# Performance work log

Measured on AMD Instinct MI355X. Metric: run time of the kernel, lower is better.

The kernel has to match this reference:

```python
import jax, jax.numpy as jnp
import numpy as np

B, P, M, H = 64, 50, 512, 64
E = 400
HYP = (1000, 2)
NEG_SLOPE = 0.01

def _leaky(x):
    return jnp.where(x >= 0, x, NEG_SLOPE * x)

def setup_inputs() -> dict:
    key = jax.random.key(0)
    ks = jax.random.split(key, 20)
    def lin(kw, kb, fi, fo):
        s = 1.0 / np.sqrt(fi)
        return (jax.random.uniform(kw, (fi, fo), jnp.float32, -s, s),
                jax.random.uniform(kb, (fo,), jnp.float32, -s, s))
    W1, b1 = lin(ks[0], ks[1], P * M, P * H)
    W2, b2 = lin(ks[2], ks[3], P * H, 2 * P * H)
    W3, b3 = lin(ks[4], ks[5], 2 * P * H, 4 * P * H)
    Wc1, bc1 = lin(ks[6], ks[7], 4 * H, 2 * H)
    Wc2, bc2 = lin(ks[8], ks[9], 2 * H, 2 * H)
    Wf1, bf1 = lin(ks[10], ks[11], 2 * H, H)
    Wf2 = jax.random.normal(ks[12], (H, int(np.prod(HYP))), jnp.float32) * 1e-7
    bf2 = jnp.full((int(np.prod(HYP)),), -10.0, jnp.float32)
    b = jax.random.normal(ks[13], (B, P, M), jnp.float32)
    edge_index = jax.random.randint(ks[14], (B, 2, E), 0, P, jnp.int32)
    return {"b": b, "edge_index": edge_index,
            "W1": W1, "b1": b1, "W2": W2, "b2": b2, "W3": W3, "b3": b3,
            "Wc1": Wc1, "bc1": bc1, "Wc2": Wc2, "bc2": bc2,
            "Wf1": Wf1, "bf1": bf1, "Wf2": Wf2, "bf2": bf2}

def _gcn(x, src, dst, norm, W, bias):
    # x: (P, Fin); symmetric-normalized sum aggregation at dst (PyG GCNConv)
    h = x @ W
    return jax.ops.segment_sum(h[src] * norm[:, None], dst, num_segments=P) + bias

def _per_sample(nodes, ei, Wc1, bc1, Wc2, bc2, Wf1, bf1, Wf2, bf2):
    loops = jnp.arange(P, dtype=ei.dtype)
    src = jnp.concatenate([ei[0], loops])
    dst = jnp.concatenate([ei[1], loops])
    deg = jax.ops.segment_sum(jnp.ones(src.shape[0], nodes.dtype), dst, num_segments=P)
    dinv = jnp.where(deg > 0, jax.lax.rsqrt(deg), 0.0)
    norm = dinv[src] * dinv[dst]
    h = _leaky(_gcn(nodes, src, dst, norm, Wc1, bc1))
    h = _leaky(_gcn(h, src, dst, norm, Wc2, bc2))
    pooled = h.mean(axis=0)                       # global_mean_pool, single graph
    z = _leaky(pooled @ Wf1 + bf1)
    z = z @ Wf2 + bf2
    return z.reshape(HYP)

def reference(b, edge_index, W1, b1, W2, b2, W3, b3, Wc1, bc1, Wc2, bc2, Wf1, bf1, Wf2, bf2):
    x = b.reshape(B, -1)
    x = _leaky(x @ W1 + b1)
    x = _leaky(x @ W2 + b2)
    x = x @ W3 + b3                               # encoder ends with Linear
    nodes = x.reshape(B, P, 4 * H)
    hyp = jax.vmap(lambda n, e: _per_sample(n, e, Wc1, bc1, Wc2, bc2, Wf1, bf1, Wf2, bf2))(nodes, edge_index)
    hyp = jnp.cumsum(hyp, axis=1)
    return jax.nn.sigmoid(hyp)
```

## Files before the change

kernel.cpp:

```cpp
#include <hip/hip_runtime.h>
#include <math.h>

typedef __attribute__((ext_vector_type(8))) short short8;
typedef __attribute__((ext_vector_type(4))) float floatx4;

constexpr int kB  = 64;
constexpr int kP  = 50;
constexpr int kE  = 400;
constexpr int kF1 = 128;
constexpr int kH  = 64;
constexpr int kNT = 2000;
constexpr int kNEDGE = kE + kP;

__device__ __forceinline__ unsigned short f2bf(float f) {
    union { float f; unsigned u; } v; v.f = f;
    unsigned u = v.u;
    u += 0x7fffu + ((u >> 16) & 1u);
    return (unsigned short)(u >> 16);
}

__device__ __forceinline__ float leakyf(float v) { return v >= 0.f ? v : 0.01f * v; }

__global__ __launch_bounds__(256) void gemm_bf16(
    const float* __restrict__ A, const float* __restrict__ W, float* __restrict__ C,
    int Mr, int N, int K, int kchunk)
{
    __shared__ unsigned short lds_a[64 * 40];
    __shared__ unsigned short lds_w[64 * 40];

    const int t  = threadIdx.x;
    const int n0 = blockIdx.x * 64;
    const int m0 = blockIdx.y * 64;
    const int k0 = blockIdx.z * kchunk;
    const int kend = k0 + kchunk;
    const bool accumulate = (gridDim.z > 1);

    const int ar = t >> 2;
    const int ac = (t & 3) * 8;
    const int wc = t & 63;
    const int wr = (t >> 6) * 8;

    const int wave = t >> 6;
    const int lane = t & 63;
    const int lrow = lane & 15;
    const int quad = lane >> 4;

    floatx4 acc[4];
#pragma unroll
    for (int c = 0; c < 4; ++c) acc[c] = (floatx4)0.f;

    for (int kk = k0; kk < kend; kk += 32) {
        {
            const float4* ap = reinterpret_cast<const float4*>(
                &A[(size_t)(m0 + ar) * K + kk + ac]);
            float4 v0 = ap[0], v1 = ap[1];
            unsigned short* dst = &lds_a[ar * 40 + ac];
            dst[0] = f2bf(v0.x); dst[1] = f2bf(v0.y);
            dst[2] = f2bf(v0.z); dst[3] = f2bf(v0.w);
            dst[4] = f2bf(v1.x); dst[5] = f2bf(v1.y);
            dst[6] = f2bf(v1.z); dst[7] = f2bf(v1.w);
        }
        {
            unsigned short* dst = &lds_w[wc * 40 + wr];
#pragma unroll
            for (int i = 0; i < 8; ++i)
                dst[i] = f2bf(W[(size_t)(kk + wr + i) * N + n0 + wc]);
        }
        __syncthreads();
        short8 af = *reinterpret_cast<const short8*>(
            &lds_a[(wave * 16 + lrow) * 40 + quad * 8]);
#pragma unroll
        for (int c = 0; c < 4; ++c) {
            short8 bf = *reinterpret_cast<const short8*>(
                &lds_w[(c * 16 + lrow) * 40 + quad * 8]);
            acc[c] = __builtin_amdgcn_mfma_f32_16x16x32_bf16(af, bf, acc[c], 0, 0, 0);
        }
        __syncthreads();
    }

#pragma unroll
    for (int c = 0; c < 4; ++c) {
#pragma unroll
        for (int r = 0; r < 4; ++r) {
            int row = m0 + wave * 16 + quad * 4 + r;
            int col = n0 + c * 16 + lrow;
            float v = acc[c][r];
            if (accumulate) atomicAdd(&C[(size_t)row * N + col], v);
            else            C[(size_t)row * N + col] = v;
        }
    }
}

__global__ __launch_bounds__(256) void bias_act_k(
    float* __restrict__ C, const float* __restrict__ bias, int total, int N, int do_leaky)
{
    int i = blockIdx.x * 256 + threadIdx.x;
    if (i >= total) return;
    float v = C[i] + bias[i % N];
    if (do_leaky) v = leakyf(v);
    C[i] = v;
}

__global__ __launch_bounds__(256) void gcn_agg(
    const float* __restrict__ hpre, const int* __restrict__ ei,
    const float* __restrict__ bias, float* __restrict__ out)
{
    __shared__ float s_agg[kP * kF1];
    __shared__ float s_deg[kP];
    __shared__ float s_dinv[kP];
    __shared__ int   s_src[kNEDGE];
    __shared__ int   s_dst[kNEDGE];
    __shared__ float s_norm[kNEDGE];

    const int s = blockIdx.x;
    const int t = threadIdx.x;

    for (int i = t; i < kP * kF1; i += 256) s_agg[i] = 0.f;
    if (t < kP) s_deg[t] = 0.f;
    __syncthreads();

    for (int e = t; e < kE; e += 256) {
        int src = ei[(size_t)s * 2 * kE + e];
        int dst = ei[(size_t)s * 2 * kE + kE + e];
        s_src[e] = src; s_dst[e] = dst;
        atomicAdd(&s_deg[dst], 1.f);
    }
    if (t < kP) {
        s_src[kE + t] = t; s_dst[kE + t] = t;
        atomicAdd(&s_deg[t], 1.f);
    }
    __syncthreads();
    if (t < kP) s_dinv[t] = rsqrtf(s_deg[t]);
    __syncthreads();
    for (int e = t; e < kNEDGE; e += 256)
        s_norm[e] = s_dinv[s_src[e]] * s_dinv[s_dst[e]];
    __syncthreads();

    const int f    = t & 127;
    const int half = t >> 7;
    for (int e = half; e < kNEDGE; e += 2) {
        float v = hpre[((size_t)s * kP + s_src[e]) * kF1 + f] * s_norm[e];
        atomicAdd(&s_agg[s_dst[e] * kF1 + f], v);
    }
    __syncthreads();

    for (int i = t; i < kP * kF1; i += 256)
        out[(size_t)s * kP * kF1 + i] = leakyf(s_agg[i] + bias[i & 127]);
}

__global__ __launch_bounds__(256) void head_k(
    const float* __restrict__ a2, const float* __restrict__ Wf1,
    const float* __restrict__ bf1, const float* __restrict__ Wf2,
    const float* __restrict__ bf2, float* __restrict__ out)
{
    __shared__ float s_pool[kF1];
    __shared__ float s_z[kH];
    __shared__ float s_t[kNT];
    __shared__ float ps0[256], ps1[256];

    const int s = blockIdx.x;
    const int t = threadIdx.x;

    if (t < kF1) {
        float acc = 0.f;
        for (int p = 0; p < kP; ++p)
            acc += a2[((size_t)s * kP + p) * kF1 + t];
        s_pool[t] = acc * (1.f / kP);
    }
    __syncthreads();
    if (t < kH) {
        float acc = bf1[t];
        for (int k = 0; k < kF1; ++k)
            acc += s_pool[k] * Wf1[k * kH + t];
        s_z[t] = leakyf(acc);
    }
    __syncthreads();
    for (int c = t; c < kNT; c += 256) {
        float acc = bf2[c];
        for (int k = 0; k < kH; ++k)
            acc += s_z[k] * Wf2[(size_t)k * kNT + c];
        s_t[c] = acc;
    }
    __syncthreads();

    float l0 = 0.f, l1 = 0.f;
    const int r0 = t * 4;
    if (r0 < 1000) {
#pragma unroll
        for (int i = 0; i < 4; ++i) {
            l0 += s_t[(r0 + i) * 2];
            l1 += s_t[(r0 + i) * 2 + 1];
        }
    }
    ps0[t] = l0; ps1[t] = l1;
    __syncthreads();
    for (int off = 1; off < 256; off <<= 1) {
        float v0 = (t >= off) ? ps0[t - off] : 0.f;
        float v1 = (t >= off) ? ps1[t - off] : 0.f;
        __syncthreads();
        ps0[t] += v0; ps1[t] += v1;
        __syncthreads();
    }
    if (r0 < 1000) {
        float run0 = ps0[t] - l0;
        float run1 = ps1[t] - l1;
        #pragma unroll
        for (int i = 0; i < 4; ++i) {
            run0 += s_t[(r0 + i) * 2];
            run1 += s_t[(r0 + i) * 2 + 1];
            out[(size_t)s * kNT + (r0 + i) * 2]     = 1.f / (1.f + expf(-run0));
            out[(size_t)s * kNT + (r0 + i) * 2 + 1] = 1.f / (1.f + expf(-run1));
        }
    }
}

extern "C" void kernel_launch(void* const* d_in, const int* in_sizes, int n_in,
                              void* d_out, int out_size, void* d_ws, size_t ws_size,
                              hipStream_t stream)
{
    const float* x   = (const float*)d_in[0];
    const int*   ei  = (const int*)d_in[1];
    const float* W1  = (const float*)d_in[2];
    const float* b1  = (const float*)d_in[3];
    const float* W2  = (const float*)d_in[4];
    const float* b2  = (const float*)d_in[5];
    const float* W3  = (const float*)d_in[6];
    const float* b3  = (const float*)d_in[7];
    const float* Wc1 = (const float*)d_in[8];
    const float* bc1 = (const float*)d_in[9];
    const float* Wc2 = (const float*)d_in[10];
    const float* bc2 = (const float*)d_in[11];
    const float* Wf1 = (const float*)d_in[12];
    const float* bf1 = (const float*)d_in[13];
    const float* Wf2 = (const float*)d_in[14];
    const float* bf2 = (const float*)d_in[15];
    float* out = (float*)d_out;

    float* ws    = (float*)d_ws;
    float* h1    = ws;
    float* h2    = h1 + 204800;
    float* nodes = h2 + 409600;
    float* g1    = nodes + 819200;
    float* a1    = g1 + 409600;
    float* g2    = a1 + 409600;
    float* a2    = g2 + 409600;

    hipMemsetAsync(h1, 0, 204800 * sizeof(float), stream);
    hipMemsetAsync(h2, 0, 409600 * sizeof(float), stream);
    hipMemsetAsync(nodes, 0, 819200 * sizeof(float), stream);

    gemm_bf16<<<dim3(3200 / 64, 1, 16), 256, 0, stream>>>(x,  W1, h1,    64, 3200, 25600, 1600);
    bias_act_k<<<(64 * 3200 + 255) / 256, 256, 0, stream>>>(h1, b1, 64 * 3200, 3200, 1);
    gemm_bf16<<<dim3(6400 / 64, 1, 8), 256, 0, stream>>>(h1, W2, h2,    64, 6400, 3200, 400);
    bias_act_k<<<(64 * 6400 + 255) / 256, 256, 0, stream>>>(h2, b2, 64 * 6400, 6400, 1);
    gemm_bf16<<<dim3(12800 / 64, 1, 8), 256, 0, stream>>>(h2, W3, nodes, 64, 12800, 6400, 800);
    bias_act_k<<<(64 * 12800 + 255) / 256, 256, 0, stream>>>(nodes, b3, 64 * 12800, 12800, 0);

    gemm_bf16<<<dim3(2, 50, 1), 256, 0, stream>>>(nodes, Wc1, g1, 3200, 128, 256, 256);
    gcn_agg<<<64, 256, 0, stream>>>(g1, ei, bc1, a1);
    gemm_bf16<<<dim3(2, 50, 1), 256, 0, stream>>>(a1, Wc2, g2, 3200, 128, 128, 128);
    gcn_agg<<<64, 256, 0, stream>>>(g2, ei, bc2, a2);

    head_k<<<64, 256, 0, stream>>>(a2, Wf1, bf1, Wf2, bf2, out);
}
```

Baseline: 1.151 ms.

## Double-buffer GEMM K-tiles, replace split-K atomics with partial-sum reduction, split GCN blocks

```diff
diff --git a/kernel.cpp b/kernel.cpp
--- a/kernel.cpp
+++ b/kernel.cpp
@@ -1,4 +1,5 @@
 #include <hip/hip_runtime.h>
+#include <hip/hip_bf16.h>
 #include <math.h>
 
 typedef __attribute__((ext_vector_type(8))) short short8;
@@ -12,33 +13,31 @@
 constexpr int kNT = 2000;
 constexpr int kNEDGE = kE + kP;
 
-__device__ __forceinline__ unsigned short f2bf(float f) {
-    union { float f; unsigned u; } v; v.f = f;
-    unsigned u = v.u;
-    u += 0x7fffu + ((u >> 16) & 1u);
-    return (unsigned short)(u >> 16);
-}
-
 __device__ __forceinline__ float leakyf(float v) { return v >= 0.f ? v : 0.01f * v; }
+
+__device__ __forceinline__ unsigned pk_bf2(float lo, float hi) {
+    union { __hip_bfloat162 h; unsigned u; } cv;
+    cv.h = __float22bfloat162_rn(make_float2(lo, hi));
+    return cv.u;
+}
 
 __global__ __launch_bounds__(256) void gemm_bf16(
     const float* __restrict__ A, const float* __restrict__ W, float* __restrict__ C,
-    int Mr, int N, int K, int kchunk)
-{
-    __shared__ unsigned short lds_a[64 * 40];
-    __shared__ unsigned short lds_w[64 * 40];
+    int N, int K, int kchunk)
+{
+    __shared__ unsigned short lds_a[2][64 * 72];
+    __shared__ unsigned short lds_w[2][64 * 72];
 
     const int t  = threadIdx.x;
     const int n0 = blockIdx.x * 64;
     const int m0 = blockIdx.y * 64;
     const int k0 = blockIdx.z * kchunk;
-    const int kend = k0 + kchunk;
-    const bool accumulate = (gridDim.z > 1);
+    const int nsteps = kchunk >> 6;
 
     const int ar = t >> 2;
-    const int ac = (t & 3) * 8;
+    const int ac = (t & 3) << 4;
     const int wc = t & 63;
-    const int wr = (t >> 6) * 8;
+    const int wk = (t >> 6) << 4;
 
     const int wave = t >> 6;
     const int lane = t & 63;
@@ -49,73 +48,107 @@
 #pragma unroll
     for (int c = 0; c < 4; ++c) acc[c] = (floatx4)0.f;
 
-    for (int kk = k0; kk < kend; kk += 32) {
-        {
-            const float4* ap = reinterpret_cast<const float4*>(
-                &A[(size_t)(m0 + ar) * K + kk + ac]);
-            float4 v0 = ap[0], v1 = ap[1];
-            unsigned short* dst = &lds_a[ar * 40 + ac];
-            dst[0] = f2bf(v0.x); dst[1] = f2bf(v0.y);
-            dst[2] = f2bf(v0.z); dst[3] = f2bf(v0.w);
-            dst[4] = f2bf(v1.x); dst[5] = f2bf(v1.y);
-            dst[6] = f2bf(v1.z); dst[7] = f2bf(v1.w);
-        }
-        {
-            unsigned short* dst = &lds_w[wc * 40 + wr];
-#pragma unroll
-            for (int i = 0; i < 8; ++i)
-                dst[i] = f2bf(W[(size_t)(kk + wr + i) * N + n0 + wc]);
-        }
+    const float* Ab = A + (size_t)(m0 + ar) * K + k0 + ac;
+    const float* Wb = W + (size_t)(k0 + wk) * N + n0 + wc;
+
+    float4 a_r[4];
+    float  w_r[16];
+
+    auto load_tile = [&](int st) {
+        const float4* ap = reinterpret_cast<const float4*>(Ab + (size_t)st * 64);
+#pragma unroll
+        for (int i = 0; i < 4; ++i) a_r[i] = ap[i];
+        const float* wp = Wb + (size_t)st * 64 * N;
+#pragma unroll
+        for (int i = 0; i < 16; ++i) w_r[i] = wp[(size_t)i * N];
+    };
+    auto stage = [&](int buf) {
+        unsigned u[8];
+#pragma unroll
+        for (int i = 0; i < 4; ++i) {
+            u[2 * i]     = pk_bf2(a_r[i].x, a_r[i].y);
+            u[2 * i + 1] = pk_bf2(a_r[i].z, a_r[i].w);
+        }
+        uint4* da = reinterpret_cast<uint4*>(&lds_a[buf][ar * 72 + ac]);
+        da[0] = make_uint4(u[0], u[1], u[2], u[3]);
+        da[1] = make_uint4(u[4], u[5], u[6], u[7]);
+#pragma unroll
+        for (int i = 0; i < 8; ++i) u[i] = pk_bf2(w_r[2 * i], w_r[2 * i + 1]);
+        uint4* dw = reinterpret_cast<uint4*>(&lds_w[buf][wc * 72 + wk]);
+        dw[0] = make_uint4(u[0], u[1], u[2], u[3]);
+        dw[1] = make_uint4(u[4], u[5], u[6], u[7]);
+    };
+    auto compute = [&](int buf) {
+#pragma unroll
+        for (int s = 0; s < 2; ++s) {
+            short8 af = *reinterpret_cast<const short8*>(
+                &lds_a[buf][(wave * 16 + lrow) * 72 + s * 32 + quad * 8]);
+#pragma unroll
+            for (int c = 0; c < 4; ++c) {
+                short8 bf = *reinterpret_cast<const short8*>(
+                    &lds_w[buf][(c * 16 + lrow) * 72 + s * 32 + quad * 8]);
+                acc[c] = __builtin_amdgcn_mfma_f32_16x16x32_bf16(af, bf, acc[c], 0, 0, 0);
+            }
+        }
+    };
+
+    load_tile(0);
+    stage(0);
+    __syncthreads();
+
+    for (int st = 0; st < nsteps; ++st) {
+        const int cur = st & 1;
+        if (st + 1 < nsteps) load_tile(st + 1);
+        compute(cur);
+        if (st + 1 < nsteps) stage(cur ^ 1);
         __syncthreads();
-        short8 af = *reinterpret_cast<const short8*>(
-            &lds_a[(wave * 16 + lrow) * 40 + quad * 8]);
-#pragma unroll
-        for (int c = 0; c < 4; ++c) {
-            short8 bf = *reinterpret_cast<const short8*>(
-                &lds_w[(c * 16 + lrow) * 40 + quad * 8]);
-            acc[c] = __builtin_amdgcn_mfma_f32_16x16x32_bf16(af, bf, acc[c], 0, 0, 0);
-        }
-        __syncthreads();
-    }
-
-#pragma unroll
-    for (int c = 0; c < 4; ++c) {
+    }
+
+    float* Cp = C + (size_t)blockIdx.z * gridDim.y * 64 * N;
+#pragma unroll
+    for (int c = 0; c < 4; ++c)
 #pragma unroll
         for (int r = 0; r < 4; ++r) {
             int row = m0 + wave * 16 + quad * 4 + r;
             int col = n0 + c * 16 + lrow;
-            float v = acc[c][r];
-            if (accumulate) atomicAdd(&C[(size_t)row * N + col], v);
-            else            C[(size_t)row * N + col] = v;
-        }
-    }
-}
-
-__global__ __launch_bounds__(256) void bias_act_k(
-    float* __restrict__ C, const float* __restrict__ bias, int total, int N, int do_leaky)
+            Cp[(size_t)row * N + col] = acc[c][r];
+        }
+}
+
+__global__ __launch_bounds__(256) void reduce_bias_act(
+    const float* __restrict__ part, const float* __restrict__ bias,
+    float* __restrict__ out, int total4, int N4, int slices, int do_leaky)
 {
     int i = blockIdx.x * 256 + threadIdx.x;
-    if (i >= total) return;
-    float v = C[i] + bias[i % N];
-    if (do_leaky) v = leakyf(v);
-    C[i] = v;
+    if (i >= total4) return;
+    const float4* p4 = reinterpret_cast<const float4*>(part);
+    float4 s = p4[i];
+    for (int z = 1; z < slices; ++z) {
+        float4 p = p4[(size_t)z * total4 + i];
+        s.x += p.x; s.y += p.y; s.z += p.z; s.w += p.w;
+    }
+    float4 b = reinterpret_cast<const float4*>(bias)[i % N4];
+    s.x += b.x; s.y += b.y; s.z += b.z; s.w += b.w;
+    if (do_leaky) { s.x = leakyf(s.x); s.y = leakyf(s.y); s.z = leakyf(s.z); s.w = leakyf(s.w); }
+    reinterpret_cast<float4*>(out)[i] = s;
 }
 
 __global__ __launch_bounds__(256) void gcn_agg(
     const float* __restrict__ hpre, const int* __restrict__ ei,
     const float* __restrict__ bias, float* __restrict__ out)
 {
-    __shared__ float s_agg[kP * kF1];
+    __shared__ float s_agg[kP * 64];
     __shared__ float s_deg[kP];
     __shared__ float s_dinv[kP];
     __shared__ int   s_src[kNEDGE];
     __shared__ int   s_dst[kNEDGE];
     __shared__ float s_norm[kNEDGE];
 
-    const int s = blockIdx.x;
-    const int t = threadIdx.x;
-
-    for (int i = t; i < kP * kF1; i += 256) s_agg[i] = 0.f;
+    const int s    = blockIdx.x >> 1;
+    const int half = blockIdx.x & 1;
+    const int t    = threadIdx.x;
+
+    for (int i = t; i < kP * 64; i += 256) s_agg[i] = 0.f;
     if (t < kP) s_deg[t] = 0.f;
     __syncthreads();
 
@@ -136,16 +169,20 @@
         s_norm[e] = s_dinv[s_src[e]] * s_dinv[s_dst[e]];
     __syncthreads();
 
-    const int f    = t & 127;
-    const int half = t >> 7;
-    for (int e = half; e < kNEDGE; e += 2) {
-        float v = hpre[((size_t)s * kP + s_src[e]) * kF1 + f] * s_norm[e];
-        atomicAdd(&s_agg[s_dst[e] * kF1 + f], v);
-    }
-    __syncthreads();
-
-    for (int i = t; i < kP * kF1; i += 256)
-        out[(size_t)s * kP * kF1 + i] = leakyf(s_agg[i] + bias[i & 127]);
+    const int f   = t & 63;
+    const int sub = t >> 6;
+    const float* hb = hpre + (size_t)s * kP * kF1 + half * 64 + f;
+    for (int e = sub; e < kNEDGE; e += 4) {
+        float v = hb[s_src[e] * kF1] * s_norm[e];
+        atomicAdd(&s_agg[s_dst[e] * 64 + f], v);
+    }
+    __syncthreads();
+
+    for (int i = t; i < kP * 64; i += 256) {
+        int p = i >> 6, ff = i & 63;
+        out[((size_t)s * kP + p) * kF1 + half * 64 + ff] =
+            leakyf(s_agg[i] + bias[half * 64 + ff]);
+    }
 }
 
 __global__ __launch_bounds__(256) void head_k(
@@ -236,8 +273,8 @@
     const float* bf2 = (const float*)d_in[15];
     float* out = (float*)d_out;
 
-    float* ws    = (float*)d_ws;
-    float* h1    = ws;
+    float* part  = (float*)d_ws;
+    float* h1    = part + 3276800;
     float* h2    = h1 + 204800;
     float* nodes = h2 + 409600;
     float* g1    = nodes + 819200;
@@ -245,21 +282,17 @@
     float* g2    = a1 + 409600;
     float* a2    = g2 + 409600;
 
-    hipMemsetAsync(h1, 0, 204800 * sizeof(float), stream);
-    hipMemsetAsync(h2, 0, 409600 * sizeof(float), stream);
-    hipMemsetAsync(nodes, 0, 819200 * sizeof(float), stream);
-
-    gemm_bf16<<<dim3(3200 / 64, 1, 16), 256, 0, stream>>>(x,  W1, h1,    64, 3200, 25600, 1600);
-    bias_act_k<<<(64 * 3200 + 255) / 256, 256, 0, stream>>>(h1, b1, 64 * 3200, 3200, 1);
-    gemm_bf16<<<dim3(6400 / 64, 1, 8), 256, 0, stream>>>(h1, W2, h2,    64, 6400, 3200, 400);
-    bias_act_k<<<(64 * 6400 + 255) / 256, 256, 0, stream>>>(h2, b2, 64 * 6400, 6400, 1);
-    gemm_bf16<<<dim3(12800 / 64, 1, 8), 256, 0, stream>>>(h2, W3, nodes, 64, 12800, 6400, 800);
-    bias_act_k<<<(64 * 12800 + 255) / 256, 256, 0, stream>>>(nodes, b3, 64 * 12800, 12800, 0);
-
-    gemm_bf16<<<dim3(2, 50, 1), 256, 0, stream>>>(nodes, Wc1, g1, 3200, 128, 256, 256);
-    gcn_agg<<<64, 256, 0, stream>>>(g1, ei, bc1, a1);
-    gemm_bf16<<<dim3(2, 50, 1), 256, 0, stream>>>(a1, Wc2, g2, 3200, 128, 128, 128);
-    gcn_agg<<<64, 256, 0, stream>>>(g2, ei, bc2, a2);
+    gemm_bf16<<<dim3(50, 1, 16), 256, 0, stream>>>(x,  W1, part, 3200, 25600, 1600);
+    reduce_bias_act<<<200, 256, 0, stream>>>(part, b1, h1,     51200,  800, 16, 1);
+    gemm_bf16<<<dim3(100, 1, 5), 256, 0, stream>>>(h1, W2, part, 6400, 3200, 640);
+    reduce_bias_act<<<400, 256, 0, stream>>>(part, b2, h2,    102400, 1600,  5, 1);
+    gemm_bf16<<<dim3(200, 1, 4), 256, 0, stream>>>(h2, W3, part, 12800, 6400, 1600);
+    reduce_bias_act<<<800, 256, 0, stream>>>(part, b3, nodes, 204800, 3200,  4, 0);
+
+    gemm_bf16<<<dim3(2, 50, 1), 256, 0, stream>>>(nodes, Wc1, g1, 128, 256, 256);
+    gcn_agg<<<128, 256, 0, stream>>>(g1, ei, bc1, a1);
+    gemm_bf16<<<dim3(2, 50, 1), 256, 0, stream>>>(a1, Wc2, g2, 128, 128, 128);
+    gcn_agg<<<128, 256, 0, stream>>>(g2, ei, bc2, a2);
 
     head_k<<<64, 256, 0, stream>>>(a2, Wf1, bf1, Wf2, bf2, out);
 }
```

Measured after the change: 1.035 ms. 1.11x faster.
